# Kernel tuning notes

Hardware: AMD Instinct MI355X
Metric: run time of the kernel (lower is better)

## Reference

```python
import jax, jax.numpy as jnp
import numpy as np


def setup_inputs() -> dict:
    key = jax.random.key(0)
    k1, k2 = jax.random.split(key)
    N, K, D = 32768, 8192, 256
    inputs = jax.random.normal(k1, (N, D), dtype=jnp.float32)
    embedding = jax.random.normal(k2, (K, D), dtype=jnp.float32)  # codebook buffer
    return {"inputs": inputs, "embedding": embedding}


def reference(inputs, embedding):
    # distances[n, k] = ||x_n||^2 + ||e_k||^2 - 2 <x_n, e_k>   (squared L2, as in torch source)
    x_sq = jnp.sum(inputs * inputs, axis=1, keepdims=True)          # [N, 1]
    e_sq = jnp.sum(embedding * embedding, axis=1)                   # [K]
    cross = inputs @ embedding.T                                    # [N, K]
    distances = x_sq + e_sq - 2.0 * cross                           # [N, K]
    encoding_indices = jnp.argmin(distances, axis=1)                # [N] int
    # torch forward returns (None, None, indices); return the tensor output
    return encoding_indices
```

## Files before the change

### kernel.cpp

```cpp
#include <hip/hip_runtime.h>

constexpr int D_DIM   = 256;
constexpr int N_ROWS  = 32768;
constexpr int K_CODES = 8192;
constexpr unsigned TQ = 58;

typedef _Float16 f16x8  __attribute__((ext_vector_type(8)));
typedef __fp16   fp16x2 __attribute__((ext_vector_type(2)));
typedef float    f32x16 __attribute__((ext_vector_type(16)));

#define MFMA32(a, b, c) __builtin_amdgcn_mfma_f32_32x32x16_f16(a, b, c, 0, 0, 0)

__device__ __forceinline__ void cvt_rtn(const float4 a, const float4 b,
                                        uint4& hi, uint4& lo) {
    float f[8] = {a.x, a.y, a.z, a.w, b.x, b.y, b.z, b.w};
    unsigned hb[8], lb[8];
#pragma unroll
    for (int i = 0; i < 8; ++i) {
        _Float16 h = (_Float16)f[i];
        _Float16 l = (_Float16)(f[i] - (float)h);
        hb[i] = __builtin_bit_cast(unsigned short, h);
        lb[i] = __builtin_bit_cast(unsigned short, l);
    }
    hi = make_uint4(hb[0] | (hb[1] << 16), hb[2] | (hb[3] << 16),
                    hb[4] | (hb[5] << 16), hb[6] | (hb[7] << 16));
    lo = make_uint4(lb[0] | (lb[1] << 16), lb[2] | (lb[3] << 16),
                    lb[4] | (lb[5] << 16), lb[6] | (lb[7] << 16));
}

__device__ __forceinline__ void cvt_granule(const float4 a, const float4 b,
                                            uint4& hi, uint4& lo) {
    fp16x2 h0 = __builtin_amdgcn_cvt_pkrtz(a.x, a.y);
    fp16x2 h1 = __builtin_amdgcn_cvt_pkrtz(a.z, a.w);
    fp16x2 h2 = __builtin_amdgcn_cvt_pkrtz(b.x, b.y);
    fp16x2 h3 = __builtin_amdgcn_cvt_pkrtz(b.z, b.w);
    fp16x2 l0 = __builtin_amdgcn_cvt_pkrtz(a.x - (float)h0.x, a.y - (float)h0.y);
    fp16x2 l1 = __builtin_amdgcn_cvt_pkrtz(a.z - (float)h1.x, a.w - (float)h1.y);
    fp16x2 l2 = __builtin_amdgcn_cvt_pkrtz(b.x - (float)h2.x, b.y - (float)h2.y);
    fp16x2 l3 = __builtin_amdgcn_cvt_pkrtz(b.z - (float)h3.x, b.w - (float)h3.y);
    hi = make_uint4(__builtin_bit_cast(unsigned, h0), __builtin_bit_cast(unsigned, h1),
                    __builtin_bit_cast(unsigned, h2), __builtin_bit_cast(unsigned, h3));
    lo = make_uint4(__builtin_bit_cast(unsigned, l0), __builtin_bit_cast(unsigned, l1),
                    __builtin_bit_cast(unsigned, l2), __builtin_bit_cast(unsigned, l3));
}

__device__ __forceinline__ void gl_lds16(const uint4* g, uint4* l) {
    __builtin_amdgcn_global_load_lds(
        (const __attribute__((address_space(1))) void*)g,
        (__attribute__((address_space(3))) void*)l, 16, 0, 0);
}

__global__ __launch_bounds__(256)
void prep_kernel(const float* __restrict__ X, const float* __restrict__ E,
                 uint4* __restrict__ Xh,
                 uint4* __restrict__ Eh, uint4* __restrict__ El,
                 float* __restrict__ esqb, int* __restrict__ cnt) {
    const int tid = threadIdx.x, bid = blockIdx.x;
    if (bid < 1024) {
#pragma unroll 1
        for (int it = 0; it < 4; ++it) {
            const int gid = bid * 1024 + it * 256 + tid;
            const int rb = gid >> 12, rem = gid & 4095;
            const int dc = rem >> 10, L = (rem >> 7) & 7, r = rem & 127;
            const float* p = X + (size_t)(rb * 128 + r) * D_DIM + dc * 64 + L * 8;
            const float4 a = *(const float4*)p, b = *(const float4*)(p + 4);
            uint4 hi, lo; cvt_rtn(a, b, hi, lo);
            Xh[gid] = hi;
        }
    } else if (bid < 1280) {
#pragma unroll 1
        for (int it = 0; it < 4; ++it) {
            const int gid = (bid - 1024) * 1024 + it * 256 + tid;
            const int cb = gid >> 13, rem = gid & 8191;
            const int dc = rem >> 11, L = (rem >> 8) & 7, c = rem & 255;
            const float* p = E + (size_t)(cb * 256 + c) * D_DIM + dc * 64 + L * 8;
            const float4 a = *(const float4*)p, b = *(const float4*)(p + 4);
            uint4 hi, lo; cvt_rtn(a, b, hi, lo);
            Eh[gid] = hi; El[gid] = lo;
        }
    } else {
        if (bid == 1280 && tid == 0) *cnt = 0;
        const int t = (bid - 1280) * 256 + tid;
        const int gw = t >> 6, lane = t & 63;
        const float4 v = ((const float4*)(E + (size_t)gw * D_DIM))[lane];
        float s = v.x * v.x + v.y * v.y + v.z * v.z + v.w * v.w;
#pragma unroll
        for (int off = 32; off; off >>= 1) s += __shfl_down(s, off, 64);
        if (lane == 0) esqb[gw] = s + 1024.0f;
    }
}

__global__ __launch_bounds__(256, 3)
void vq_pass1(const uint4* __restrict__ Xh, const uint4* __restrict__ Eh,
              const float* __restrict__ esqb, uint2* __restrict__ res) {
    __shared__ uint4 sXh[1024];
    __shared__ uint4 sEh[1024];
    __shared__ uint2 slot[2][128];

    const int tid  = threadIdx.x;
    const int lane = tid & 63, wv = tid >> 6, wr = wv >> 1, wc = wv & 1;
    const int l31  = lane & 31, lh = lane >> 5;
    const int wbase = wv << 6;
    const int bx = blockIdx.x, strip = blockIdx.y;
    const int cs0 = strip * 2048;

    const uint4* Xhb = Xh + bx * 4096;

    unsigned best[2][16], best2[2][16];
#pragma unroll
    for (int ti = 0; ti < 2; ++ti)
#pragma unroll
        for (int r = 0; r < 16; ++r) { best[ti][r] = 0xFFFFFFFFu; best2[ti][r] = 0xFFFFFFFFu; }

    f32x16 acc[2][2];

#pragma unroll 1
    for (int ct = 0; ct < 16; ++ct) {
        const int cb   = strip * 8 + (ct >> 1);
        const int coff = (ct & 1) * 128;
        const uint4* Ehb = Eh + (size_t)cb * 8192;

#pragma unroll
        for (int ti = 0; ti < 2; ++ti)
#pragma unroll
            for (int tj = 0; tj < 2; ++tj)
#pragma unroll
                for (int i = 0; i < 16; ++i) acc[ti][tj][i] = 0.0f;

#pragma unroll 1
        for (int dc = 0; dc < 4; ++dc) {
            __syncthreads();
#pragma unroll
            for (int i = 0; i < 4; ++i)
                gl_lds16(Xhb + dc * 1024 + i * 256 + tid, &sXh[i * 256 + wbase]);
#pragma unroll
            for (int i = 0; i < 4; ++i) {
                const int idx = wv * 4 + i, L = idx >> 1, ch = idx & 1;
                gl_lds16(Ehb + dc * 2048 + L * 256 + coff + ch * 64 + lane,
                         &sEh[L * 128 + ch * 64]);
            }
            __syncthreads();

#pragma unroll
            for (int s = 0; s < 4; ++s) {
                const int L = s * 2 + lh;
                f16x8 a0[2], b0[2];
#pragma unroll
                for (int ti = 0; ti < 2; ++ti)
                    a0[ti] = __builtin_bit_cast(f16x8, sXh[L * 128 + wr * 64 + ti * 32 + l31]);
#pragma unroll
                for (int tj = 0; tj < 2; ++tj)
                    b0[tj] = __builtin_bit_cast(f16x8, sEh[L * 128 + wc * 64 + tj * 32 + l31]);
#pragma unroll
                for (int ti = 0; ti < 2; ++ti)
#pragma unroll
                    for (int tj = 0; tj < 2; ++tj)
                        acc[ti][tj] = MFMA32(a0[ti], b0[tj], acc[ti][tj]);
            }
        }

#pragma unroll
        for (int tj = 0; tj < 2; ++tj) {
            const int code = cs0 + ct * 128 + wc * 64 + tj * 32 + l31;
            const float eb128 = esqb[code] * 128.0f;
#pragma unroll
            for (int ti = 0; ti < 2; ++ti)
#pragma unroll
                for (int r = 0; r < 16; ++r) {
                    const float dq = fmaf(-256.0f, acc[ti][tj][r], eb128);
                    const unsigned q   = (unsigned)dq;
                    const unsigned key = (q << 13) + (unsigned)code;
                    const unsigned t   = key > best[ti][r] ? key : best[ti][r];
                    best2[ti][r] = best2[ti][r] < t ? best2[ti][r] : t;
                    best[ti][r]  = best[ti][r] < key ? best[ti][r] : key;
                }
        }
    }

#pragma unroll
    for (int ti = 0; ti < 2; ++ti)
#pragma unroll
        for (int r = 0; r < 16; ++r) {
            unsigned b1 = best[ti][r], b2 = best2[ti][r];
#pragma unroll
            for (int m = 16; m >= 1; m >>= 1) {
                const unsigned o1 = (unsigned)__shfl_xor((int)b1, m, 32);
                const unsigned o2 = (unsigned)__shfl_xor((int)b2, m, 32);
                const unsigned t  = b1 > o1 ? b1 : o1;
                b1 = b1 < o1 ? b1 : o1;
                const unsigned m2 = b2 < o2 ? b2 : o2;
                b2 = m2 < t ? m2 : t;
            }
            if (l31 == 0) {
                const int row = wr * 64 + ti * 32 + (r & 3) + 8 * (r >> 2) + 4 * lh;
                slot[wc][row] = make_uint2(b1, b2);
            }
        }

    __syncthreads();
    if (tid < 128) {
        const uint2 A = slot[0][tid], B = slot[1][tid];
        const unsigned t  = A.x > B.x ? A.x : B.x;
        const unsigned b1 = A.x < B.x ? A.x : B.x;
        const unsigned m2 = A.y < B.y ? A.y : B.y;
        const unsigned b2 = m2 < t ? m2 : t;
        res[(size_t)strip * N_ROWS + bx * 128 + tid] = make_uint2(b1, b2);
    }
}

__global__ void merge_kernel(const uint2* __restrict__ res,
                             unsigned long long* __restrict__ res0,
                             int* __restrict__ out,
                             int* __restrict__ cnt, int* __restrict__ list) {
    const int row = blockIdx.x * 256 + threadIdx.x;
    unsigned b1 = 0xFFFFFFFFu, b2 = 0xFFFFFFFFu;
#pragma unroll
    for (int s = 0; s < 4; ++s) {
        const uint2 v = res[(size_t)s * N_ROWS + row];
        const unsigned t = b1 > v.x ? b1 : v.x;
        b1 = b1 < v.x ? b1 : v.x;
        const unsigned m2 = b2 < v.y ? b2 : v.y;
        b2 = m2 < t ? m2 : t;
    }
    out[row] = (int)(b1 & 8191u);
    if ((b2 >> 13) - (b1 >> 13) < TQ) {
        const int p = atomicAdd(cnt, 1);
        list[p] = row;
        res0[row] = ~0ull;
    }
}

__global__ __launch_bounds__(256, 1)
void refine_kernel(const float* __restrict__ X,
                   const uint4* __restrict__ Eh, const uint4* __restrict__ El,
                   const float* __restrict__ esqb, const int* __restrict__ cnt,
                   const int* __restrict__ list, unsigned long long* __restrict__ res0) {
    __shared__ int  rows_s[32];
    __shared__ uint4 sAh[1024], sAl[1024];

    const int n = *cnt;
    const int base = blockIdx.x * 32;
    if (base >= n) return;
    const int tid = threadIdx.x;
    if (tid < 32) { const int j = base + tid; rows_s[tid] = list[j < n ? j : base]; }
    __syncthreads();

#pragma unroll
    for (int jj = 0; jj < 4; ++jj) {
        const int gg = jj * 256 + tid, Lg = gg >> 5, rr = gg & 31;
        const int row = rows_s[rr];
        const float* p = X + (size_t)row * D_DIM + Lg * 8;
        const float4 a = *(const float4*)p, b = *(const float4*)(p + 4);
        uint4 hi, lo; cvt_rtn(a, b, hi, lo);
        sAh[Lg * 32 + rr] = hi; sAl[Lg * 32 + rr] = lo;
    }
    __syncthreads();

    const int lane = tid & 63, wv = tid >> 6, l31 = lane & 31, lh = lane >> 5;
    const int cbase = blockIdx.y * 1024 + wv * 256;

    float bestv[16]; int besti[16];
#pragma unroll
    for (int r = 0; r < 16; ++r) { bestv[r] = 3.0e38f; besti[r] = 0; }

#pragma unroll 1
    for (int ps = 0; ps < 2; ++ps) {
        const int c0 = cbase + ps * 128;
        f32x16 acc[4];
#pragma unroll
        for (int tj = 0; tj < 4; ++tj)
#pragma unroll
            for (int i = 0; i < 16; ++i) acc[tj][i] = 0.0f;

#pragma unroll
        for (int ks = 0; ks < 16; ++ks) {
            const int Lg = ks * 2 + lh;
            f16x8 b0[4], b1[4];
#pragma unroll
            for (int tj = 0; tj < 4; ++tj) {
                const int c = c0 + tj * 32 + l31;
                const int eg = (c >> 8) * 8192 + (Lg >> 3) * 2048 + (Lg & 7) * 256 + (c & 255);
                b0[tj] = __builtin_bit_cast(f16x8, Eh[eg]);
                b1[tj] = __builtin_bit_cast(f16x8, El[eg]);
            }
            const f16x8 a0 = __builtin_bit_cast(f16x8, sAh[Lg * 32 + l31]);
            const f16x8 a1 = __builtin_bit_cast(f16x8, sAl[Lg * 32 + l31]);
#pragma unroll
            for (int tj = 0; tj < 4; ++tj) acc[tj] = MFMA32(a1, b0[tj], acc[tj]);
#pragma unroll
            for (int tj = 0; tj < 4; ++tj) acc[tj] = MFMA32(a0, b1[tj], acc[tj]);
#pragma unroll
            for (int tj = 0; tj < 4; ++tj) acc[tj] = MFMA32(a0, b0[tj], acc[tj]);
        }

#pragma unroll
        for (int tj = 0; tj < 4; ++tj) {
            const int c = c0 + tj * 32 + l31;
            const float eb = esqb[c];
#pragma unroll
            for (int r = 0; r < 16; ++r) {
                const float dv = fmaf(-2.0f, acc[tj][r], eb);
                if (dv < bestv[r]) { bestv[r] = dv; besti[r] = c; }
            }
        }
    }

#pragma unroll
    for (int r = 0; r < 16; ++r) {
        float v = bestv[r]; int bi = besti[r];
#pragma unroll
        for (int m = 16; m >= 1; m >>= 1) {
            const float ov = __shfl_xor(v, m, 32);
            const int   oi = __shfl_xor(bi, m, 32);
            if (ov < v || (ov == v && oi < bi)) { v = ov; bi = oi; }
        }
        if (l31 == 0) {
            const int rl = (r & 3) + 8 * (r >> 2) + 4 * lh;
            atomicMin(&res0[rows_s[rl]],
                      ((unsigned long long)__float_as_uint(v) << 32) | (unsigned)bi);
        }
    }
}

__global__ void finalize_kernel(const unsigned long long* __restrict__ res0,
                                const int* __restrict__ cnt, const int* __restrict__ list,
                                int* __restrict__ out) {
    const int i = blockIdx.x * 256 + threadIdx.x;
    if (i < *cnt) {
        const int row = list[i];
        out[row] = (int)(res0[row] & 0xFFFFFFFFull);
    }
}

__global__ void prologue_fb(const float* __restrict__ E, float* __restrict__ esqb,
                            unsigned long long* __restrict__ packed) {
    const int t = blockIdx.x * 256 + threadIdx.x;
    if (t < N_ROWS) packed[t] = ~0ull;
    const int gw = t >> 6, lane = t & 63;
    const float4 v = ((const float4*)(E + (size_t)gw * D_DIM))[lane];
    float s = v.x * v.x + v.y * v.y + v.z * v.z + v.w * v.w;
#pragma unroll
    for (int off = 32; off; off >>= 1) s += __shfl_down(s, off, 64);
    if (lane == 0) esqb[gw] = s + 1024.0f;
}

__global__ __launch_bounds__(256, 2)
void vq_mfma_fallback(const float* __restrict__ X, const float* __restrict__ E,
                      const float* __restrict__ esqb,
                      unsigned long long* __restrict__ packed) {
    __shared__ uint4 fXh[128 * 8], fXl[128 * 8];
    __shared__ uint4 fEh[128 * 8], fEl[128 * 8];
    __shared__ float fEsq[2048];

    const int tid  = threadIdx.x;
    const int lane = tid & 63;
    const int wv   = tid >> 6;
    const int wr   = wv >> 1, wc = wv & 1;
    const int l31  = lane & 31;
    const int lh   = lane >> 5;
    const int row0 = blockIdx.x * 128;
    const int cs0  = blockIdx.y * 2048;

#pragma unroll
    for (int i = 0; i < 8; ++i) fEsq[tid + 256 * i] = esqb[cs0 + tid + 256 * i];

    const int sr = tid >> 3, sg = tid & 7;

    float best[2][16]; int bidx[2][16];
#pragma unroll
    for (int ti = 0; ti < 2; ++ti)
#pragma unroll
        for (int r = 0; r < 16; ++r) { best[ti][r] = 3.0e38f; bidx[ti][r] = 0; }

    f32x16 acc[2][2];

#pragma unroll 1
    for (int ct = 0; ct < 16; ++ct) {
#pragma unroll
        for (int ti = 0; ti < 2; ++ti)
#pragma unroll
            for (int tj = 0; tj < 2; ++tj)
#pragma unroll
                for (int i = 0; i < 16; ++i) acc[ti][tj][i] = 0.0f;

#pragma unroll 1
        for (int dc = 0; dc < 4; ++dc) {
            __syncthreads();
#pragma unroll
            for (int i = 0; i < 4; ++i) {
                const int r = 32 * i + sr;
                const float* p = X + (size_t)(row0 + r) * D_DIM + dc * 64 + sg * 8;
                const float4 a = *(const float4*)p, b = *(const float4*)(p + 4);
                uint4 hi, lo; cvt_granule(a, b, hi, lo);
                const int o = r * 8 + (sg ^ (r & 7));
                fXh[o] = hi; fXl[o] = lo;
            }
#pragma unroll
            for (int i = 0; i < 4; ++i) {
                const int r = 32 * i + sr;
                const float* p = E + (size_t)(cs0 + ct * 128 + r) * D_DIM + dc * 64 + sg * 8;
                const float4 a = *(const float4*)p, b = *(const float4*)(p + 4);
                uint4 hi, lo; cvt_granule(a, b, hi, lo);
                const int o = r * 8 + (sg ^ (r & 7));
                fEh[o] = hi; fEl[o] = lo;
            }
            __syncthreads();

#pragma unroll
            for (int s = 0; s < 4; ++s) {
                const int gi = s * 2 + lh;
                f16x8 axh[2], axl[2], beh[2], bel[2];
#pragma unroll
                for (int ti = 0; ti < 2; ++ti) {
                    const int r = wr * 64 + ti * 32 + l31;
                    const int o = r * 8 + (gi ^ (r & 7));
                    axh[ti] = __builtin_bit_cast(f16x8, fXh[o]);
                    axl[ti] = __builtin_bit_cast(f16x8, fXl[o]);
                }
#pragma unroll
                for (int tj = 0; tj < 2; ++tj) {
                    const int c = wc * 64 + tj * 32 + l31;
                    const int o = c * 8 + (gi ^ (c & 7));
                    beh[tj] = __builtin_bit_cast(f16x8, fEh[o]);
                    bel[tj] = __builtin_bit_cast(f16x8, fEl[o]);
                }
#pragma unroll
                for (int ti = 0; ti < 2; ++ti)
#pragma unroll
                    for (int tj = 0; tj < 2; ++tj) {
                        acc[ti][tj] = MFMA32(axl[ti], beh[tj], acc[ti][tj]);
                        acc[ti][tj] = MFMA32(axh[ti], bel[tj], acc[ti][tj]);
                        acc[ti][tj] = MFMA32(axh[ti], beh[tj], acc[ti][tj]);
                    }
            }
        }

#pragma unroll
        for (int tj = 0; tj < 2; ++tj) {
            const int cloc = ct * 128 + wc * 64 + tj * 32 + l31;
            const float eb = fEsq[cloc];
            const int  code = cs0 + cloc;
#pragma unroll
            for (int ti = 0; ti < 2; ++ti)
#pragma unroll
                for (int r = 0; r < 16; ++r) {
                    const float dv = fmaf(-2.0f, acc[ti][tj][r], eb);
                    if (dv < best[ti][r]) { best[ti][r] = dv; bidx[ti][r] = code; }
                }
        }
    }

#pragma unroll
    for (int ti = 0; ti < 2; ++ti)
#pragma unroll
        for (int r = 0; r < 16; ++r) {
            float b = best[ti][r]; int bi = bidx[ti][r];
#pragma unroll
            for (int m = 16; m >= 1; m >>= 1) {
                const float ov = __shfl_xor(b, m, 32);
                const int   oi = __shfl_xor(bi, m, 32);
                if (ov < b || (ov == b && oi < bi)) { b = ov; bi = oi; }
            }
            if (l31 == 0) {
                const int row = row0 + wr * 64 + ti * 32 + (r & 3) + 8 * (r >> 2) + 4 * lh;
                const unsigned long long p =
                    ((unsigned long long)__float_as_uint(b) << 32) | (unsigned)bi;
                atomicMin(&packed[row], p);
            }
        }
}

__global__ void finish_fb(const unsigned long long* __restrict__ packed,
                          int* __restrict__ out) {
    const int i = blockIdx.x * 256 + threadIdx.x;
    out[i] = (int)(unsigned)(packed[i] & 0xffffffffull);
}

extern "C" void kernel_launch(void* const* d_in, const int* in_sizes, int n_in,
                              void* d_out, int out_size, void* d_ws, size_t ws_size,
                              hipStream_t stream) {
    const float* X = (const float*)d_in[0];
    const float* E = (const float*)d_in[1];
    char* ws = (char*)d_ws;
    int* out = (int*)d_out;

    float* esqb = (float*)ws;
    uint2* res  = (uint2*)(ws + 32768);
    unsigned long long* res0 = (unsigned long long*)(ws + 1081344);
    int* cnt  = (int*)(ws + 1343488);
    int* list = (int*)(ws + 1343504);
    const size_t base = 1572864;
    const size_t szX  = (size_t)N_ROWS * D_DIM * 2;
    const size_t szE  = (size_t)K_CODES * D_DIM * 2;
    const size_t need = base + szX + 2 * szE;

    if (ws_size >= need) {
        uint4* Xh = (uint4*)(ws + base);
        uint4* Eh = (uint4*)(ws + base + szX);
        uint4* El = (uint4*)(ws + base + szX + szE);
        prep_kernel<<<dim3(3328), dim3(256), 0, stream>>>(X, E, Xh, Eh, El, esqb, cnt);
        vq_pass1<<<dim3(N_ROWS / 128, 4), dim3(256), 0, stream>>>(Xh, Eh, esqb, res);
        merge_kernel<<<dim3(N_ROWS / 256), dim3(256), 0, stream>>>(res, res0, out, cnt, list);
        refine_kernel<<<dim3(1024, 8), dim3(256), 0, stream>>>(X, Eh, El, esqb,
                                                               cnt, list, res0);
        finalize_kernel<<<dim3(N_ROWS / 256), dim3(256), 0, stream>>>(res0, cnt, list, out);
    } else {
        unsigned long long* packed = (unsigned long long*)(ws + 32768);
        prologue_fb<<<dim3(2048), dim3(256), 0, stream>>>(E, esqb, packed);
        vq_mfma_fallback<<<dim3(N_ROWS / 128, 4), dim3(256), 0, stream>>>(X, E, esqb, packed);
        finish_fb<<<dim3(N_ROWS / 256), dim3(256), 0, stream>>>(packed, out);
    }
}
```

Measured before the change: 379.6 us.

## Keep full X tile resident in LDS and stream codebook fragments from global

Pass 1 now loads the whole 128x256 fp16 X tile into LDS once per block. It drops the per-dc staging of X and E with its two barriers per chunk. Codebook B fragments are read straight from global memory into registers, which removes E's LDS traffic and all per-iteration syncs. The prep layout is flattened to a linear Lg index to match, and pass 2 indexing is updated accordingly. LDS per block grows to 64KB, so occupancy is lowered to 2 blocks per CU, and global-load latency is exposed in the MFMA loop.

```diff
diff --git a/kernel.cpp b/kernel.cpp
--- a/kernel.cpp
+++ b/kernel.cpp
@@ -61,8 +61,8 @@
         for (int it = 0; it < 4; ++it) {
             const int gid = bid * 1024 + it * 256 + tid;
             const int rb = gid >> 12, rem = gid & 4095;
-            const int dc = rem >> 10, L = (rem >> 7) & 7, r = rem & 127;
-            const float* p = X + (size_t)(rb * 128 + r) * D_DIM + dc * 64 + L * 8;
+            const int Lg = rem >> 7, r = rem & 127;
+            const float* p = X + (size_t)(rb * 128 + r) * D_DIM + Lg * 8;
             const float4 a = *(const float4*)p, b = *(const float4*)(p + 4);
             uint4 hi, lo; cvt_rtn(a, b, hi, lo);
             Xh[gid] = hi;
@@ -72,8 +72,8 @@
         for (int it = 0; it < 4; ++it) {
             const int gid = (bid - 1024) * 1024 + it * 256 + tid;
             const int cb = gid >> 13, rem = gid & 8191;
-            const int dc = rem >> 11, L = (rem >> 8) & 7, c = rem & 255;
-            const float* p = E + (size_t)(cb * 256 + c) * D_DIM + dc * 64 + L * 8;
+            const int Lg = rem >> 8, c = rem & 255;
+            const float* p = E + (size_t)(cb * 256 + c) * D_DIM + Lg * 8;
             const float4 a = *(const float4*)p, b = *(const float4*)(p + 4);
             uint4 hi, lo; cvt_rtn(a, b, hi, lo);
             Eh[gid] = hi; El[gid] = lo;
@@ -90,11 +90,10 @@
     }
 }
 
-__global__ __launch_bounds__(256, 3)
+__global__ __launch_bounds__(256, 2)
 void vq_pass1(const uint4* __restrict__ Xh, const uint4* __restrict__ Eh,
               const float* __restrict__ esqb, uint2* __restrict__ res) {
-    __shared__ uint4 sXh[1024];
-    __shared__ uint4 sEh[1024];
+    __shared__ uint4 sXh[4096];
     __shared__ uint2 slot[2][128];
 
     const int tid  = threadIdx.x;
@@ -106,6 +105,11 @@
 
     const uint4* Xhb = Xh + bx * 4096;
 
+#pragma unroll
+    for (int i = 0; i < 16; ++i)
+        gl_lds16(Xhb + i * 256 + tid, &sXh[i * 256 + wbase]);
+    __syncthreads();
+
     unsigned best[2][16], best2[2][16];
 #pragma unroll
     for (int ti = 0; ti < 2; ++ti)
@@ -113,12 +117,12 @@
         for (int r = 0; r < 16; ++r) { best[ti][r] = 0xFFFFFFFFu; best2[ti][r] = 0xFFFFFFFFu; }
 
     f32x16 acc[2][2];
+    const int arow = wr * 64 + l31;
 
 #pragma unroll 1
     for (int ct = 0; ct < 16; ++ct) {
-        const int cb   = strip * 8 + (ct >> 1);
-        const int coff = (ct & 1) * 128;
-        const uint4* Ehb = Eh + (size_t)cb * 8192;
+        const uint4* __restrict__ Eb =
+            Eh + (size_t)(strip * 8 + (ct >> 1)) * 8192 + (ct & 1) * 128 + wc * 64 + l31;
 
 #pragma unroll
         for (int ti = 0; ti < 2; ++ti)
@@ -127,36 +131,17 @@
 #pragma unroll
                 for (int i = 0; i < 16; ++i) acc[ti][tj][i] = 0.0f;
 
-#pragma unroll 1
-        for (int dc = 0; dc < 4; ++dc) {
-            __syncthreads();
-#pragma unroll
-            for (int i = 0; i < 4; ++i)
-                gl_lds16(Xhb + dc * 1024 + i * 256 + tid, &sXh[i * 256 + wbase]);
-#pragma unroll
-            for (int i = 0; i < 4; ++i) {
-                const int idx = wv * 4 + i, L = idx >> 1, ch = idx & 1;
-                gl_lds16(Ehb + dc * 2048 + L * 256 + coff + ch * 64 + lane,
-                         &sEh[L * 128 + ch * 64]);
-            }
-            __syncthreads();
-
-#pragma unroll
-            for (int s = 0; s < 4; ++s) {
-                const int L = s * 2 + lh;
-                f16x8 a0[2], b0[2];
-#pragma unroll
-                for (int ti = 0; ti < 2; ++ti)
-                    a0[ti] = __builtin_bit_cast(f16x8, sXh[L * 128 + wr * 64 + ti * 32 + l31]);
-#pragma unroll
-                for (int tj = 0; tj < 2; ++tj)
-                    b0[tj] = __builtin_bit_cast(f16x8, sEh[L * 128 + wc * 64 + tj * 32 + l31]);
-#pragma unroll
-                for (int ti = 0; ti < 2; ++ti)
-#pragma unroll
-                    for (int tj = 0; tj < 2; ++tj)
-                        acc[ti][tj] = MFMA32(a0[ti], b0[tj], acc[ti][tj]);
-            }
+#pragma unroll 4
+        for (int k = 0; k < 16; ++k) {
+            const int Lg = k * 2 + lh;
+            const f16x8 b0 = __builtin_bit_cast(f16x8, Eb[Lg * 256]);
+            const f16x8 b1 = __builtin_bit_cast(f16x8, Eb[Lg * 256 + 32]);
+            const f16x8 a0 = __builtin_bit_cast(f16x8, sXh[Lg * 128 + arow]);
+            const f16x8 a1 = __builtin_bit_cast(f16x8, sXh[Lg * 128 + arow + 32]);
+            acc[0][0] = MFMA32(a0, b0, acc[0][0]);
+            acc[0][1] = MFMA32(a0, b1, acc[0][1]);
+            acc[1][0] = MFMA32(a1, b0, acc[1][0]);
+            acc[1][1] = MFMA32(a1, b1, acc[1][1]);
         }
 
 #pragma unroll
@@ -279,7 +264,7 @@
 #pragma unroll
             for (int tj = 0; tj < 4; ++tj) {
                 const int c = c0 + tj * 32 + l31;
-                const int eg = (c >> 8) * 8192 + (Lg >> 3) * 2048 + (Lg & 7) * 256 + (c & 255);
+                const int eg = (c >> 8) * 8192 + Lg * 256 + (c & 255);
                 b0[tj] = __builtin_bit_cast(f16x8, Eh[eg]);
                 b1[tj] = __builtin_bit_cast(f16x8, El[eg]);
             }
```

After: 361.9 us. 4.7% less time.
